# Kernel tuning notes

Measured on AMD Instinct MI355X. Metric: run time of the kernel, lower is better.

## Reference

```python
import jax, jax.numpy as jnp
import numpy as np

D = 1024      # d_model
E = 8         # initial_experts
H = 4 * D     # expert FFN hidden
CAP_F = 1.25  # capacity_factor
VOCAB = 256


def setup_inputs() -> dict:
    key = jax.random.key(0)
    ks = jax.random.split(key, 10)
    w = lambda k, shape, s: jax.random.normal(k, shape, jnp.float32) * s
    return dict(
        byte_seq=jax.random.randint(ks[0], (4, 2048), 0, VOCAB, jnp.int32),
        emb=w(ks[1], (VOCAB, D), 0.02),
        Wp=w(ks[2], (D, D), 1.0 / np.sqrt(D)), bp=jnp.zeros((D,), jnp.float32),
        Wg=w(ks[3], (D, D), 1.0 / np.sqrt(D)), bg=jnp.zeros((D,), jnp.float32),
        Wr=w(ks[4], (D, E), 1.0 / np.sqrt(D)), br=jnp.zeros((E,), jnp.float32),
        W1=w(ks[5], (E, D, H), 1.0 / np.sqrt(D)), b1=jnp.zeros((E, H), jnp.float32),
        W2=w(ks[6], (E, H, D), 1.0 / np.sqrt(H)), b2=jnp.zeros((E, D), jnp.float32),
        Wh=w(ks[7], (D, VOCAB), 1.0 / np.sqrt(D)), bh=jnp.zeros((VOCAB,), jnp.float32),
    )


def reference(byte_seq, emb, Wp, bp, Wg, bg, Wr, br, W1, b1, W2, b2, Wh, bh):
    # ---- byte embedding ----
    x = emb[byte_seq]                                 # [B,T,D]
    B, T, _ = x.shape

    # ---- SSM core: precompute input projections, scan only the recurrence ----
    px = x @ Wp + bp                                   # [B,T,D]
    gx = jax.nn.sigmoid(x @ Wg + bg)                   # [B,T,D]

    def step(state, inp):
        p, g = inp
        state = jnp.tanh(p + state)
        return state, g * state

    s0 = jnp.zeros((B, D), x.dtype)
    next_state, ys = jax.lax.scan(step, s0, (px.transpose(1, 0, 2), gx.transpose(1, 0, 2)))
    y = ys.transpose(1, 0, 2)                          # [B,T,D]

    # ---- capacity-limited top-1 MoE routing ----
    xf = y.reshape(-1, D)                              # [N,D]
    N = xf.shape[0]
    probs = jax.nn.softmax(xf @ Wr + br, axis=-1)      # [N,E]
    top = jnp.argmax(probs, axis=-1)                   # [N]
    onehot = jax.nn.one_hot(top, E, dtype=xf.dtype)    # [N,E]
    pos = jnp.cumsum(onehot, axis=0) * onehot          # 1-based slot within expert
    capacity = int(CAP_F * N / E)
    keep = (pos > 0) & (pos <= capacity)               # [N,E] tokens within capacity
    gate = jnp.take_along_axis(probs, top[:, None], axis=-1)[:, 0]  # [N]
    scale = gate * keep.any(axis=-1).astype(xf.dtype)

    # grouped expert FFN (fixed small loop over experts, masked combine)
    out = jnp.zeros_like(xf)
    for e in range(E):
        h = jax.nn.gelu(xf @ W1[e] + b1[e])            # [N,H]
        oe = h @ W2[e] + b2[e]                         # [N,D]
        out = out + oe * keep[:, e].astype(xf.dtype)[:, None]
    out = out * scale[:, None]

    entropy_loss = -jnp.mean(jnp.sum(probs * jnp.log(probs + 1e-9), axis=-1))
    expert_counts = jnp.sum(onehot, axis=0)

    logits = out.reshape(B, T, D) @ Wh + bh            # [B,T,256]
    return logits, next_state, entropy_loss, expert_counts
```

## Files before the change

kernel.cpp:

```cpp
#include <hip/hip_runtime.h>
#include <hip/hip_bf16.h>
#include <cstdint>
#include <cstddef>

#define AS1 __attribute__((address_space(1)))
#define AS3 __attribute__((address_space(3)))

typedef __hip_bfloat16 bf16;
typedef float f32x4 __attribute__((ext_vector_type(4)));
typedef short bf16x8 __attribute__((ext_vector_type(8)));

#define B_     4
#define T_     2048
#define D_     1024
#define E_     8
#define H_     4096
#define NTOK   8192
#define CAP    1280
#define VOCAB_ 256

static constexpr size_t OFF_PG    = 0;
static constexpr size_t OFF_Y     = 2097152;
static constexpr size_t OFF_TOP   = 35651584;
static constexpr size_t OFF_GATE  = 35684352;
static constexpr size_t OFF_ENT   = 35717120;
static constexpr size_t OFF_CNT   = 35749888;
static constexpr size_t OFF_CKEPT = 35750144;
static constexpr size_t OFF_SLOT  = 35750400;
static constexpr size_t OFF_XE    = 35791360;
static constexpr size_t OFF_HE    = 56762880;
static constexpr size_t OFF_WT    = 140648960;
static constexpr size_t OFF_WHT   = 207757824;
static constexpr size_t OFF_OUTB  = 208282112;

#define LOGITS_OFF 0
#define NS_OFF     2097152
#define ENT_OFF    2101248
#define CNT_OFF    2101249

__device__ __forceinline__ void gll16(const void* g, void* l) {
  __builtin_amdgcn_global_load_lds((AS1 const void*)g, (AS3 void*)l, 16, 0, 0);
}
__device__ __forceinline__ unsigned short f2bu(float f) {
  bf16 h = __float2bfloat16(f);
  return __builtin_bit_cast(unsigned short, h);
}
__device__ __forceinline__ float bu2f(unsigned short u) {
  unsigned int x = ((unsigned int)u) << 16;
  return __builtin_bit_cast(float, x);
}
__device__ __forceinline__ float fast_tanh(float z) {
  float e2 = __expf(z + z);
  return fmaf(-2.f, __builtin_amdgcn_rcpf(e2 + 1.f), 1.f);
}

__global__ __launch_bounds__(256) void slv_embproj_part(
    const float* __restrict__ emb, const float* __restrict__ Wp,
    const float* __restrict__ Wg,
    float* __restrict__ Ppart, float* __restrict__ Gpart) {
  __shared__ float embT[128][9];
  int rb = blockIdx.x, kc = blockIdx.y;
  int r0 = rb * 8, k0 = kc * 128;
  int tid = threadIdx.x;
  int c = tid * 4;
  {
    int i4 = tid * 4;
    int r = i4 >> 7, kb = i4 & 127;
    f32x4 v = *reinterpret_cast<const f32x4*>(emb + (size_t)(r0 + r) * D_ + k0 + kb);
    embT[kb + 0][r] = v.x; embT[kb + 1][r] = v.y;
    embT[kb + 2][r] = v.z; embT[kb + 3][r] = v.w;
  }
  __syncthreads();
  f32x4 aP[8] = {}, aG[8] = {};
  #pragma unroll 4
  for (int kk = 0; kk < 128; ++kk) {
    f32x4 wp = *reinterpret_cast<const f32x4*>(Wp + (size_t)(k0 + kk) * D_ + c);
    f32x4 wg = *reinterpret_cast<const f32x4*>(Wg + (size_t)(k0 + kk) * D_ + c);
    #pragma unroll
    for (int r = 0; r < 8; ++r) {
      float e = embT[kk][r];
      aP[r] += e * wp;
      aG[r] += e * wg;
    }
  }
  #pragma unroll
  for (int r = 0; r < 8; ++r) {
    size_t o = ((size_t)kc * 256 + r0 + r) * D_ + c;
    *reinterpret_cast<f32x4*>(Ppart + o) = aP[r];
    *reinterpret_cast<f32x4*>(Gpart + o) = aG[r];
  }
}

__global__ __launch_bounds__(256) void slv_embproj_reduce(
    const float* __restrict__ Ppart, const float* __restrict__ Gpart,
    const float* __restrict__ bp, const float* __restrict__ bg,
    float2* __restrict__ PG) {
  int i = blockIdx.x * 256 + threadIdx.x;
  int r = i >> 8;
  int c = (i & 255) * 4;
  f32x4 sp = {}, sg = {};
  #pragma unroll
  for (int kc = 0; kc < 8; ++kc) {
    size_t o = ((size_t)kc * 256 + r) * D_ + c;
    sp += *reinterpret_cast<const f32x4*>(Ppart + o);
    sg += *reinterpret_cast<const f32x4*>(Gpart + o);
  }
  sp += *reinterpret_cast<const f32x4*>(bp + c);
  sg += *reinterpret_cast<const f32x4*>(bg + c);
  f32x4 g;
  g.x = 1.f / (1.f + __expf(-sg.x));
  g.y = 1.f / (1.f + __expf(-sg.y));
  g.z = 1.f / (1.f + __expf(-sg.z));
  g.w = 1.f / (1.f + __expf(-sg.w));
  f32x4 st0 = { sp.x, g.x, sp.y, g.y };
  f32x4 st1 = { sp.z, g.z, sp.w, g.w };
  f32x4* dst = reinterpret_cast<f32x4*>(PG + (size_t)r * D_ + c);
  dst[0] = st0; dst[1] = st1;
}

__global__ __launch_bounds__(256) void slv_gatherpg(
    const int* __restrict__ bytes, const float2* __restrict__ PG,
    float2* __restrict__ pg_seq) {
  int t0 = blockIdx.x * 16;
  __shared__ int bl[16];
  if (threadIdx.x < 16) bl[threadIdx.x] = bytes[t0 + threadIdx.x];
  __syncthreads();
  int c = threadIdx.x * 4;
  #pragma unroll 4
  for (int u = 0; u < 16; ++u) {
    const f32x4* src = (const f32x4*)(PG + (size_t)bl[u] * D_ + c);
    f32x4* dst = (f32x4*)(pg_seq + (size_t)(t0 + u) * D_ + c);
    f32x4 v0 = src[0], v1 = src[1];
    dst[0] = v0; dst[1] = v1;
  }
}

#define SU 16
__global__ __launch_bounds__(64, 1) void slv_scan(
    const float2* __restrict__ pg_seq,
    float* __restrict__ y, float* __restrict__ ns) {
  int b = blockIdx.x >> 4;
  int d = (blockIdx.x & 15) * 64 + threadIdx.x;
  const float2* pp = pg_seq + (size_t)b * T_ * D_ + d;
  float* yp = y + (size_t)b * T_ * D_ + d;
  float2 pA[SU], pB[SU];
  #pragma unroll
  for (int u = 0; u < SU; ++u) pA[u] = pp[(size_t)u * D_];
  float s = 0.f;
  for (int t0 = 0; t0 < T_; t0 += 2 * SU) {
    #pragma unroll
    for (int u = 0; u < SU; ++u) pB[u] = pp[(size_t)(t0 + SU + u) * D_];
    #pragma unroll
    for (int u = 0; u < SU; ++u) {
      s = fast_tanh(pA[u].x + s);
      yp[(size_t)(t0 + u) * D_] = pA[u].y * s;
    }
    if (t0 + 2 * SU < T_) {
      #pragma unroll
      for (int u = 0; u < SU; ++u) pA[u] = pp[(size_t)(t0 + 2 * SU + u) * D_];
    }
    #pragma unroll
    for (int u = 0; u < SU; ++u) {
      s = fast_tanh(pB[u].x + s);
      yp[(size_t)(t0 + SU + u) * D_] = pB[u].y * s;
    }
  }
  ns[b * D_ + d] = s;
}

__global__ __launch_bounds__(256) void slv_router(
    const float* __restrict__ y, const float* __restrict__ Wr, const float* __restrict__ br,
    int* __restrict__ top, float* __restrict__ gate, float* __restrict__ entTok,
    int* __restrict__ countsInt) {
  int wave = threadIdx.x >> 6, lane = threadIdx.x & 63;
  int tok = blockIdx.x * 4 + wave;
  const float* yr = y + (size_t)tok * D_;
  float acc[E_];
  #pragma unroll
  for (int e = 0; e < E_; ++e) acc[e] = 0.f;
  for (int i = 0; i < 16; ++i) {
    int d = i * 64 + lane;
    float v = yr[d];
    const float4* w = (const float4*)(Wr + d * E_);
    float4 w0 = w[0], w1 = w[1];
    acc[0] = fmaf(v, w0.x, acc[0]); acc[1] = fmaf(v, w0.y, acc[1]);
    acc[2] = fmaf(v, w0.z, acc[2]); acc[3] = fmaf(v, w0.w, acc[3]);
    acc[4] = fmaf(v, w1.x, acc[4]); acc[5] = fmaf(v, w1.y, acc[5]);
    acc[6] = fmaf(v, w1.z, acc[6]); acc[7] = fmaf(v, w1.w, acc[7]);
  }
  #pragma unroll
  for (int off = 32; off; off >>= 1)
    #pragma unroll
    for (int e = 0; e < E_; ++e) acc[e] += __shfl_xor(acc[e], off);
  if (lane == 0) {
    float l[E_], p[E_];
    float mx = -1e30f;
    #pragma unroll
    for (int e = 0; e < E_; ++e) { l[e] = acc[e] + br[e]; mx = fmaxf(mx, l[e]); }
    float sum = 0.f;
    #pragma unroll
    for (int e = 0; e < E_; ++e) { p[e] = expf(l[e] - mx); sum += p[e]; }
    float inv = 1.f / sum;
    int bestE = 0; float bestP = -1.f; float ent = 0.f;
    #pragma unroll
    for (int e = 0; e < E_; ++e) {
      float pe = p[e] * inv;
      ent += pe * logf(pe + 1e-9f);
      if (pe > bestP) { bestP = pe; bestE = e; }
    }
    top[tok] = bestE; gate[tok] = bestP; entTok[tok] = ent;
    atomicAdd(&countsInt[bestE], 1);
  }
}

__global__ __launch_bounds__(256) void slv_capacity(
    const int* __restrict__ top, int* __restrict__ slotTok, int* __restrict__ cntKept) {
  __shared__ unsigned char tops[NTOK];
  __shared__ unsigned int wt[4][4];
  int tid = threadIdx.x, lane = tid & 63, w = tid >> 6;
  for (int i = tid; i < NTOK; i += 256) tops[i] = (unsigned char)top[i];
  __syncthreads();
  unsigned int c0 = 0, c1 = 0, c2 = 0, c3 = 0;
  int n0 = tid * 32;
  for (int i = 0; i < 32; ++i) {
    int v = tops[n0 + i];
    unsigned inc = 1u << ((v & 1) << 4);
    int hi = v >> 1;
    if (hi == 0) c0 += inc;
    else if (hi == 1) c1 += inc;
    else if (hi == 2) c2 += inc;
    else c3 += inc;
  }
  unsigned int s0 = c0, s1 = c1, s2 = c2, s3 = c3;
  #pragma unroll
  for (int off = 1; off < 64; off <<= 1) {
    unsigned int t0 = (unsigned)__shfl_up((int)s0, off);
    unsigned int t1 = (unsigned)__shfl_up((int)s1, off);
    unsigned int t2 = (unsigned)__shfl_up((int)s2, off);
    unsigned int t3 = (unsigned)__shfl_up((int)s3, off);
    if (lane >= off) { s0 += t0; s1 += t1; s2 += t2; s3 += t3; }
  }
  if (lane == 63) { wt[w][0] = s0; wt[w][1] = s1; wt[w][2] = s2; wt[w][3] = s3; }
  __syncthreads();
  unsigned int p0 = 0, p1 = 0, p2 = 0, p3 = 0;
  for (int i = 0; i < w; ++i) { p0 += wt[i][0]; p1 += wt[i][1]; p2 += wt[i][2]; p3 += wt[i][3]; }
  unsigned int e0 = s0 - c0 + p0, e1 = s1 - c1 + p1, e2 = s2 - c2 + p2, e3 = s3 - c3 + p3;
  int base[E_];
  base[0] = e0 & 0xffff; base[1] = e0 >> 16;
  base[2] = e1 & 0xffff; base[3] = e1 >> 16;
  base[4] = e2 & 0xffff; base[5] = e2 >> 16;
  base[6] = e3 & 0xffff; base[7] = e3 >> 16;
  if (tid == 0) {
    unsigned int t0t = wt[0][0] + wt[1][0] + wt[2][0] + wt[3][0];
    unsigned int t1t = wt[0][1] + wt[1][1] + wt[2][1] + wt[3][1];
    unsigned int t2t = wt[0][2] + wt[1][2] + wt[2][2] + wt[3][2];
    unsigned int t3t = wt[0][3] + wt[1][3] + wt[2][3] + wt[3][3];
    cntKept[0] = min((int)(t0t & 0xffff), CAP); cntKept[1] = min((int)(t0t >> 16), CAP);
    cntKept[2] = min((int)(t1t & 0xffff), CAP); cntKept[3] = min((int)(t1t >> 16), CAP);
    cntKept[4] = min((int)(t2t & 0xffff), CAP); cntKept[5] = min((int)(t2t >> 16), CAP);
    cntKept[6] = min((int)(t3t & 0xffff), CAP); cntKept[7] = min((int)(t3t >> 16), CAP);
  }
  for (int i = 0; i < 32; ++i) {
    int n = n0 + i;
    int v = tops[n];
    #pragma unroll
    for (int e = 0; e < E_; ++e) {
      if (v == e) {
        int r = base[e]++;
        if (r < CAP) slotTok[e * CAP + r] = n;
      }
    }
  }
}

__global__ __launch_bounds__(256) void slv_gather(
    const float* __restrict__ y, const int* __restrict__ slotTok,
    const int* __restrict__ cntKept, unsigned short* __restrict__ Xe) {
  int slot = blockIdx.x;
  int e = slot / CAP, r = slot % CAP;
  int c4 = threadIdx.x * 4;
  ushort4 o;
  if (r < cntKept[e]) {
    int tok = slotTok[slot];
    float4 v = *(const float4*)(y + (size_t)tok * D_ + c4);
    o.x = f2bu(v.x); o.y = f2bu(v.y); o.z = f2bu(v.z); o.w = f2bu(v.w);
  } else {
    o.x = 0; o.y = 0; o.z = 0; o.w = 0;
  }
  *(ushort4*)(Xe + (size_t)slot * D_ + c4) = o;
}

__global__ __launch_bounds__(256) void slv_transpose(
    const float* __restrict__ in, bf16* __restrict__ out, int R, int C) {
  __shared__ float tile[64][65];
  size_t mat = (size_t)blockIdx.z * R * C;
  int c0 = blockIdx.x * 64, r0 = blockIdx.y * 64;
  int tid = threadIdx.x;
  #pragma unroll
  for (int j = 0; j < 16; ++j) {
    int idx = j * 256 + tid; int r = idx >> 6, c = idx & 63;
    tile[r][c] = in[mat + (size_t)(r0 + r) * C + c0 + c];
  }
  __syncthreads();
  #pragma unroll
  for (int j = 0; j < 4; ++j) {
    int lin = j * 256 + tid;
    int cc = lin >> 4;
    int rr = (lin & 15) * 4;
    ushort4 v;
    v.x = f2bu(tile[rr + 0][cc]); v.y = f2bu(tile[rr + 1][cc]);
    v.z = f2bu(tile[rr + 2][cc]); v.w = f2bu(tile[rr + 3][cc]);
    *(ushort4*)((unsigned short*)out + mat + (size_t)(c0 + cc) * R + r0 + rr) = v;
  }
}

__device__ __forceinline__ void gemm_core(
    const char* ga, const char* gb, int K, bf16* As, bf16* Bs,
    f32x4 (&acc)[4][4], int wave, int lane, int wr, int wc) {
  const int Krow = K * 2;
  for (int ks = 0; ks < K; ks += 64) {
    #pragma unroll
    for (int rnd = 0; rnd < 4; ++rnd) {
      int chunk = rnd * 4 + wave;
      int o = chunk * 1024 + lane * 16;
      int row = o >> 7, col = o & 127;
      int scol = col ^ ((row & 7) << 4);
      size_t gofs = (size_t)row * Krow + (size_t)ks * 2 + scol;
      gll16(ga + gofs, (char*)As + chunk * 1024);
      gll16(gb + gofs, (char*)Bs + chunk * 1024);
    }
    __syncthreads();
    #pragma unroll
    for (int kk = 0; kk < 2; ++kk) {
      bf16x8 a[4], b[4];
      int koff = kk * 64 + ((lane >> 4) << 4);
      #pragma unroll
      for (int m = 0; m < 4; ++m) {
        int row = wr * 64 + m * 16 + (lane & 15);
        int sc = koff ^ ((row & 7) << 4);
        a[m] = *(const bf16x8*)((const char*)As + row * 128 + sc);
      }
      #pragma unroll
      for (int n = 0; n < 4; ++n) {
        int row = wc * 64 + n * 16 + (lane & 15);
        int sc = koff ^ ((row & 7) << 4);
        b[n] = *(const bf16x8*)((const char*)Bs + row * 128 + sc);
      }
      #pragma unroll
      for (int m = 0; m < 4; ++m)
        #pragma unroll
        for (int n = 0; n < 4; ++n)
          acc[m][n] = __builtin_amdgcn_mfma_f32_16x16x32_bf16(a[m], b[n], acc[m][n], 0, 0, 0);
    }
    __syncthreads();
  }
}

__device__ __forceinline__ void gemm256_8p(
    const char* ga, const char* gb, size_t krow, size_t kbyte0, int NH,
    char* lds, int tid, int lane, int wr, int wc, f32x4 (&acc)[8][4]) {
  auto STG = [&](int h, int r) {
    int o = (r & 1) * 8192 + tid * 16;
    int l = o >> 7, rem = o & 127;
    int rem2 = rem ^ ((l & 7) << 4);
    int row = 2 * l + (rem2 >> 6);
    int kb = rem2 & 63;
    const char* g = (r < 2) ? ga : gb;
    size_t gofs = (size_t)row * krow + kbyte0 + (size_t)h * 64 + kb;
    gll16(g + gofs, lds + (h & 3) * 32768 + ((r < 2) ? 0 : 16384) + o);
  };
  int l15 = lane & 15;
  int lhalf = l15 >> 1;
  int aoff = (((lane & 1) << 6) | ((lane >> 4) << 4)) ^ (lhalf << 4);
  STG(0, 0); STG(0, 1); STG(0, 2); STG(0, 3);
  STG(1, 0); STG(1, 1); STG(1, 2); STG(1, 3);
  STG(2, 0); STG(2, 1); STG(2, 2); STG(2, 3);
  asm volatile("s_waitcnt vmcnt(8)" ::: "memory");
  __builtin_amdgcn_s_barrier();
  for (int h = 0; h < NH; ++h) {
    const char* Ab = lds + (h & 3) * 32768;
    const char* Bb = Ab + 16384;
    bf16x8 a[4], b[4];
    #pragma unroll
    for (int n = 0; n < 4; ++n)
      b[n] = *(const bf16x8*)(Bb + 128 * (wc * 32 + n * 8 + lhalf) + aoff);
    #pragma unroll
    for (int m = 0; m < 4; ++m)
      a[m] = *(const bf16x8*)(Ab + 128 * (wr * 64 + m * 8 + lhalf) + aoff);
    if (h + 3 < NH) { STG(h + 3, 0); STG(h + 3, 1); }
    __builtin_amdgcn_s_barrier();
    asm volatile("s_waitcnt lgkmcnt(0)" ::: "memory");
    __builtin_amdgcn_sched_barrier(0);
    __builtin_amdgcn_s_setprio(1);
    #pragma unroll
    for (int m = 0; m < 4; ++m)
      #pragma unroll
      for (int n = 0; n < 4; ++n)
        acc[m][n] = __builtin_amdgcn_mfma_f32_16x16x32_bf16(a[m], b[n], acc[m][n], 0, 0, 0);
    __builtin_amdgcn_s_setprio(0);
    __builtin_amdgcn_s_barrier();
    #pragma unroll
    for (int m = 0; m < 4; ++m)
      a[m] = *(const bf16x8*)(Ab + 128 * (wr * 64 + (m + 4) * 8 + lhalf) + aoff);
    if (h + 3 < NH) { STG(h + 3, 2); STG(h + 3, 3); }
    if (h + 3 <= NH - 1)      asm volatile("s_waitcnt vmcnt(8)" ::: "memory");
    else if (h + 2 == NH - 1) asm volatile("s_waitcnt vmcnt(4)" ::: "memory");
    else if (h + 1 == NH - 1) asm volatile("s_waitcnt vmcnt(0)" ::: "memory");
    __builtin_amdgcn_s_barrier();
    asm volatile("s_waitcnt lgkmcnt(0)" ::: "memory");
    __builtin_amdgcn_sched_barrier(0);
    __builtin_amdgcn_s_setprio(1);
    #pragma unroll
    for (int m = 0; m < 4; ++m)
      #pragma unroll
      for (int n = 0; n < 4; ++n)
        acc[m + 4][n] = __builtin_amdgcn_mfma_f32_16x16x32_bf16(a[m], b[n], acc[m + 4][n], 0, 0, 0);
    __builtin_amdgcn_s_setprio(0);
    __builtin_amdgcn_s_barrier();
  }
}

__global__ __launch_bounds__(512, 2) void slv_ffn1_g(
    const bf16* __restrict__ Xe, const bf16* __restrict__ W1t, const float* __restrict__ b1,
    const int* __restrict__ cntKept, unsigned short* __restrict__ He) {
  int e = blockIdx.z, mt = blockIdx.y, nt = blockIdx.x;
  if (mt * 256 >= cntKept[e]) return;
  extern __shared__ char lds[];
  int tid = threadIdx.x, wave = tid >> 6, lane = tid & 63;
  int wr = wave >> 2, wc = wave & 3;
  const char* ga = (const char*)(Xe + ((size_t)e * CAP + mt * 256) * D_);
  const char* gb = (const char*)(W1t + ((size_t)e * H_ + nt * 256) * D_);
  f32x4 acc[8][4] = {};
  gemm256_8p(ga, gb, (size_t)D_ * 2, 0, D_ / 32, lds, tid, lane, wr, wc, acc);
  size_t slot0 = (size_t)e * CAP + mt * 256;
  int colb = nt * 256 + wc * 64;
  #pragma unroll
  for (int m = 0; m < 8; ++m) {
    int trow0 = wr * 128 + m * 16 + ((lane >> 4) << 2);
    #pragma unroll
    for (int n = 0; n < 4; ++n) {
      int col = colb + n * 16 + (lane & 15);
      float bias = b1[e * H_ + col];
      #pragma unroll
      for (int r = 0; r < 4; ++r) {
        float x = acc[m][n][r] + bias;
        float t = fast_tanh(0.7978845608028654f * (x + 0.044715f * x * x * x));
        float gel = 0.5f * x * (1.f + t);
        He[(slot0 + trow0 + r) * (size_t)H_ + col] = f2bu(gel);
      }
    }
  }
}

__global__ __launch_bounds__(512, 2) void slv_ffn2_part(
    const bf16* __restrict__ He, const bf16* __restrict__ W2t,
    const int* __restrict__ cntKept,
    unsigned short* __restrict__ part0, unsigned short* __restrict__ part1) {
  int ez = blockIdx.z;
  int e = ez >> 1, s = ez & 1;
  int mt = blockIdx.y, nt = blockIdx.x;
  if (mt * 256 >= cntKept[e]) return;
  extern __shared__ char lds[];
  int tid = threadIdx.x, wave = tid >> 6, lane = tid & 63;
  int wr = wave >> 2, wc = wave & 3;
  const char* ga = (const char*)(He + ((size_t)e * CAP + mt * 256) * H_);
  const char* gb = (const char*)(W2t + ((size_t)e * D_ + nt * 256) * H_);
  f32x4 acc[8][4] = {};
  gemm256_8p(ga, gb, (size_t)H_ * 2, (size_t)s * 2048 * 2, 2048 / 32,
             lds, tid, lane, wr, wc, acc);
  unsigned short* part = s ? part1 : part0;
  size_t slot0 = (size_t)e * CAP + mt * 256;
  int colb = nt * 256 + wc * 64;
  #pragma unroll
  for (int m = 0; m < 8; ++m) {
    int trow0 = wr * 128 + m * 16 + ((lane >> 4) << 2);
    #pragma unroll
    for (int n = 0; n < 4; ++n) {
      int col = colb + n * 16 + (lane & 15);
      #pragma unroll
      for (int r = 0; r < 4; ++r)
        part[(slot0 + trow0 + r) * (size_t)D_ + col] = f2bu(acc[m][n][r]);
    }
  }
}

__global__ __launch_bounds__(256) void slv_ffn2_reduce(
    const unsigned short* __restrict__ part0, const unsigned short* __restrict__ part1,
    const float* __restrict__ b2, const int* __restrict__ cntKept,
    const int* __restrict__ slotTok, const float* __restrict__ gate,
    unsigned short* __restrict__ outb) {
  int slot = blockIdx.x;
  int e = slot / CAP, r = slot % CAP;
  if (r >= cntKept[e]) return;
  int tok = slotTok[slot];
  float sc = gate[tok];
  int c4 = threadIdx.x * 4;
  ushort4 p0 = *(const ushort4*)(part0 + (size_t)slot * D_ + c4);
  ushort4 p1 = *(const ushort4*)(part1 + (size_t)slot * D_ + c4);
  const float4 bb = *(const float4*)(b2 + e * D_ + c4);
  ushort4 o;
  o.x = f2bu((bu2f(p0.x) + bu2f(p1.x) + bb.x) * sc);
  o.y = f2bu((bu2f(p0.y) + bu2f(p1.y) + bb.y) * sc);
  o.z = f2bu((bu2f(p0.z) + bu2f(p1.z) + bb.z) * sc);
  o.w = f2bu((bu2f(p0.w) + bu2f(p1.w) + bb.w) * sc);
  *(ushort4*)(outb + (size_t)tok * D_ + c4) = o;
}

__global__ __launch_bounds__(256) void slv_head(
    const bf16* __restrict__ outb, const bf16* __restrict__ Wht, const float* __restrict__ bh,
    float* __restrict__ logits) {
  int nt = blockIdx.x, mt = blockIdx.y;
  __shared__ __align__(16) bf16 As[128 * 64], Bs[128 * 64];
  int tid = threadIdx.x, wave = tid >> 6, lane = tid & 63;
  int wr = wave >> 1, wc = wave & 1;
  const char* ga = (const char*)(outb + (size_t)mt * 128 * D_);
  const char* gb = (const char*)(Wht + (size_t)nt * 128 * D_);
  f32x4 acc[4][4] = {};
  gemm_core(ga, gb, D_, As, Bs, acc, wave, lane, wr, wc);
  int colb = nt * 128 + wc * 64;
  #pragma unroll
  for (int m = 0; m < 4; ++m) {
    int trow0 = wr * 64 + m * 16 + ((lane >> 4) << 2);
    #pragma unroll
    for (int n = 0; n < 4; ++n) {
      int col = colb + n * 16 + (lane & 15);
      float bias = bh[col];
      #pragma unroll
      for (int r = 0; r < 4; ++r) {
        int row = mt * 128 + trow0 + r;
        logits[(size_t)row * VOCAB_ + col] = acc[m][n][r] + bias;
      }
    }
  }
}

__global__ __launch_bounds__(256) void slv_finalize(
    const float* __restrict__ entTok, const int* __restrict__ countsInt,
    float* __restrict__ out) {
  __shared__ float red[256];
  int tid = threadIdx.x;
  float s = 0.f;
  for (int i = tid; i < NTOK; i += 256) s += entTok[i];
  red[tid] = s;
  __syncthreads();
  for (int off = 128; off; off >>= 1) {
    if (tid < off) red[tid] += red[tid + off];
    __syncthreads();
  }
  if (tid == 0) out[ENT_OFF] = -red[0] / (float)NTOK;
  if (tid < E_) out[CNT_OFF + tid] = (float)countsInt[tid];
}

extern "C" void kernel_launch(void* const* d_in, const int* in_sizes, int n_in,
                              void* d_out, int out_size, void* d_ws, size_t ws_size,
                              hipStream_t stream) {
  (void)in_sizes; (void)n_in; (void)out_size; (void)ws_size;
  const int*   byte_seq = (const int*)d_in[0];
  const float* emb = (const float*)d_in[1];
  const float* Wp  = (const float*)d_in[2];
  const float* bp  = (const float*)d_in[3];
  const float* Wg  = (const float*)d_in[4];
  const float* bg  = (const float*)d_in[5];
  const float* Wr  = (const float*)d_in[6];
  const float* br  = (const float*)d_in[7];
  const float* W1  = (const float*)d_in[8];
  const float* b1  = (const float*)d_in[9];
  const float* W2  = (const float*)d_in[10];
  const float* b2  = (const float*)d_in[11];
  const float* Wh  = (const float*)d_in[12];
  const float* bh  = (const float*)d_in[13];
  float* out = (float*)d_out;

  char* ws = (char*)d_ws;
  float2* PG      = (float2*)(ws + OFF_PG);
  float* y        = (float*)(ws + OFF_Y);
  int*   top      = (int*)(ws + OFF_TOP);
  float* gate     = (float*)(ws + OFF_GATE);
  float* entTok   = (float*)(ws + OFF_ENT);
  int*   countsInt= (int*)(ws + OFF_CNT);
  int*   cntKept  = (int*)(ws + OFF_CKEPT);
  int*   slotTok  = (int*)(ws + OFF_SLOT);
  unsigned short* Xe  = (unsigned short*)(ws + OFF_XE);
  unsigned short* He  = (unsigned short*)(ws + OFF_HE);
  bf16*  Wt       = (bf16*)(ws + OFF_WT);
  bf16*  Wht      = (bf16*)(ws + OFF_WHT);
  unsigned short* outb = (unsigned short*)(ws + OFF_OUTB);
  float*  Ppart   = (float*)(ws + OFF_HE);
  float*  Gpart   = (float*)(ws + OFF_HE + 8388608);
  float2* pg_seq  = (float2*)(ws + OFF_HE);
  unsigned short* part0 = (unsigned short*)(ws + OFF_Y);
  unsigned short* part1 = (unsigned short*)(ws + OFF_XE);

  hipFuncSetAttribute(reinterpret_cast<const void*>(slv_ffn1_g),
                      hipFuncAttributeMaxDynamicSharedMemorySize, 131072);
  hipFuncSetAttribute(reinterpret_cast<const void*>(slv_ffn2_part),
                      hipFuncAttributeMaxDynamicSharedMemorySize, 131072);

  hipMemsetAsync(countsInt, 0, E_ * sizeof(int), stream);
  hipMemsetAsync(outb, 0, (size_t)NTOK * D_ * 2, stream);

  slv_embproj_part<<<dim3(32, 8), 256, 0, stream>>>(emb, Wp, Wg, Ppart, Gpart);
  slv_embproj_reduce<<<256, 256, 0, stream>>>(Ppart, Gpart, bp, bg, PG);
  slv_gatherpg<<<NTOK / 16, 256, 0, stream>>>(byte_seq, PG, pg_seq);
  slv_scan<<<64, 64, 0, stream>>>(pg_seq, y, out + NS_OFF);
  slv_router<<<NTOK / 4, 256, 0, stream>>>(y, Wr, br, top, gate, entTok, countsInt);
  slv_capacity<<<1, 256, 0, stream>>>(top, slotTok, cntKept);
  slv_gather<<<E_ * CAP, 256, 0, stream>>>(y, slotTok, cntKept, Xe);

  slv_transpose<<<dim3(4, 16, 1), 256, 0, stream>>>(Wh, Wht, 1024, 256);
  slv_transpose<<<dim3(64, 16, 8), 256, 0, stream>>>(W1, Wt, 1024, 4096);
  slv_ffn1_g<<<dim3(16, 5, 8), 512, 131072, stream>>>((const bf16*)Xe, Wt, b1, cntKept, He);
  slv_transpose<<<dim3(16, 64, 8), 256, 0, stream>>>(W2, Wt, 4096, 1024);
  slv_ffn2_part<<<dim3(4, 5, 16), 512, 131072, stream>>>((const bf16*)He, Wt, cntKept, part0, part1);
  slv_ffn2_reduce<<<E_ * CAP, 256, 0, stream>>>(part0, part1, b2, cntKept, slotTok, gate, outb);
  slv_head<<<dim3(2, 64), 256, 0, stream>>>((const bf16*)outb, Wht, bh, out + LOGITS_OFF);
  slv_finalize<<<1, 256, 0, stream>>>(entTok, countsInt, out);
}
```

Baseline: 570.5 us.

## Overlap weight transposes with scan and shrink expert GEMM tiles to 128 rows

Folds the Wh and W1 transposes into the scan launch as extra blocks, so the idle GPU during the latency-bound 16-block sequential scan does transpose work in parallel. The scan now uses 16 blocks of 256 threads instead of 64 blocks of 64. The expert FFN GEMMs move from 256x256 tiles with a 4-stage buffer to 128x256 tiles with a 3-stage buffer and less LDS, allowing more blocks per CU and finer skipping of empty capacity rows. The trade-off is less data reuse per tile, and the scan's wave layout changes, which may affect its latency.

```diff
diff --git a/kernel.cpp b/kernel.cpp
--- a/kernel.cpp
+++ b/kernel.cpp
@@ -135,12 +135,48 @@
   }
 }
 
+__device__ __forceinline__ void transpose_tile(
+    const float* __restrict__ in, bf16* __restrict__ out, int R, int C,
+    int bx, int by, int bz, int tid) {
+  __shared__ float tile[64][65];
+  size_t mat = (size_t)bz * R * C;
+  int c0 = bx * 64, r0 = by * 64;
+  #pragma unroll
+  for (int j = 0; j < 16; ++j) {
+    int idx = j * 256 + tid; int r = idx >> 6, c = idx & 63;
+    tile[r][c] = in[mat + (size_t)(r0 + r) * C + c0 + c];
+  }
+  __syncthreads();
+  #pragma unroll
+  for (int j = 0; j < 4; ++j) {
+    int lin = j * 256 + tid;
+    int cc = lin >> 4;
+    int rr = (lin & 15) * 4;
+    ushort4 v;
+    v.x = f2bu(tile[rr + 0][cc]); v.y = f2bu(tile[rr + 1][cc]);
+    v.z = f2bu(tile[rr + 2][cc]); v.w = f2bu(tile[rr + 3][cc]);
+    *(ushort4*)((unsigned short*)out + mat + (size_t)(c0 + cc) * R + r0 + rr) = v;
+  }
+}
+
 #define SU 16
-__global__ __launch_bounds__(64, 1) void slv_scan(
-    const float2* __restrict__ pg_seq,
-    float* __restrict__ y, float* __restrict__ ns) {
-  int b = blockIdx.x >> 4;
-  int d = (blockIdx.x & 15) * 64 + threadIdx.x;
+__global__ __launch_bounds__(256, 1) void slv_scan_trans(
+    const float2* __restrict__ pg_seq, float* __restrict__ y, float* __restrict__ ns,
+    const float* __restrict__ W1, bf16* __restrict__ W1t,
+    const float* __restrict__ Wh, bf16* __restrict__ Wht) {
+  int bid = blockIdx.x, tid = threadIdx.x;
+  if (bid >= 16) {
+    if (bid < 80) {
+      int blk = bid - 16;
+      transpose_tile(Wh, Wht, 1024, 256, blk & 3, blk >> 2, 0, tid);
+    } else {
+      int blk = bid - 80;
+      transpose_tile(W1, W1t, 1024, 4096, blk & 63, (blk >> 6) & 15, blk >> 10, tid);
+    }
+    return;
+  }
+  int b = bid >> 2;
+  int d = (bid & 3) * 256 + tid;
   const float2* pp = pg_seq + (size_t)b * T_ * D_ + d;
   float* yp = y + (size_t)b * T_ * D_ + d;
   float2 pA[SU], pB[SU];
@@ -292,26 +328,7 @@
 
 __global__ __launch_bounds__(256) void slv_transpose(
     const float* __restrict__ in, bf16* __restrict__ out, int R, int C) {
-  __shared__ float tile[64][65];
-  size_t mat = (size_t)blockIdx.z * R * C;
-  int c0 = blockIdx.x * 64, r0 = blockIdx.y * 64;
-  int tid = threadIdx.x;
-  #pragma unroll
-  for (int j = 0; j < 16; ++j) {
-    int idx = j * 256 + tid; int r = idx >> 6, c = idx & 63;
-    tile[r][c] = in[mat + (size_t)(r0 + r) * C + c0 + c];
-  }
-  __syncthreads();
-  #pragma unroll
-  for (int j = 0; j < 4; ++j) {
-    int lin = j * 256 + tid;
-    int cc = lin >> 4;
-    int rr = (lin & 15) * 4;
-    ushort4 v;
-    v.x = f2bu(tile[rr + 0][cc]); v.y = f2bu(tile[rr + 1][cc]);
-    v.z = f2bu(tile[rr + 2][cc]); v.w = f2bu(tile[rr + 3][cc]);
-    *(ushort4*)((unsigned short*)out + mat + (size_t)(c0 + cc) * R + r0 + rr) = v;
-  }
+  transpose_tile(in, out, R, C, blockIdx.x, blockIdx.y, blockIdx.z, threadIdx.x);
 }
 
 __device__ __forceinline__ void gemm_core(
@@ -356,39 +373,40 @@
   }
 }
 
-__device__ __forceinline__ void gemm256_8p(
+__device__ __forceinline__ void gemm_hp(
     const char* ga, const char* gb, size_t krow, size_t kbyte0, int NH,
-    char* lds, int tid, int lane, int wr, int wc, f32x4 (&acc)[8][4]) {
+    char* lds, int tid, int lane, int wr, int wc, f32x4 (&acc)[4][4]) {
   auto STG = [&](int h, int r) {
-    int o = (r & 1) * 8192 + tid * 16;
+    int o = (r == 0) ? (tid * 16) : ((r - 1) * 8192 + tid * 16);
     int l = o >> 7, rem = o & 127;
     int rem2 = rem ^ ((l & 7) << 4);
     int row = 2 * l + (rem2 >> 6);
     int kb = rem2 & 63;
-    const char* g = (r < 2) ? ga : gb;
+    const char* g = (r == 0) ? ga : gb;
     size_t gofs = (size_t)row * krow + kbyte0 + (size_t)h * 64 + kb;
-    gll16(g + gofs, lds + (h & 3) * 32768 + ((r < 2) ? 0 : 16384) + o);
+    gll16(g + gofs, lds + (h % 3) * 24576 + ((r == 0) ? 0 : 8192) + o);
   };
-  int l15 = lane & 15;
-  int lhalf = l15 >> 1;
+  int lhalf = (lane & 15) >> 1;
   int aoff = (((lane & 1) << 6) | ((lane >> 4) << 4)) ^ (lhalf << 4);
-  STG(0, 0); STG(0, 1); STG(0, 2); STG(0, 3);
-  STG(1, 0); STG(1, 1); STG(1, 2); STG(1, 3);
-  STG(2, 0); STG(2, 1); STG(2, 2); STG(2, 3);
-  asm volatile("s_waitcnt vmcnt(8)" ::: "memory");
+  STG(0, 0); STG(0, 1); STG(0, 2);
+  STG(1, 0); STG(1, 1); STG(1, 2);
+  asm volatile("s_waitcnt vmcnt(3)" ::: "memory");
   __builtin_amdgcn_s_barrier();
   for (int h = 0; h < NH; ++h) {
-    const char* Ab = lds + (h & 3) * 32768;
-    const char* Bb = Ab + 16384;
+    const char* Ab = lds + (h % 3) * 24576;
+    const char* Bb = Ab + 8192;
     bf16x8 a[4], b[4];
+    #pragma unroll
+    for (int m = 0; m < 4; ++m)
+      a[m] = *(const bf16x8*)(Ab + 128 * (wr * 32 + m * 8 + lhalf) + aoff);
     #pragma unroll
     for (int n = 0; n < 4; ++n)
       b[n] = *(const bf16x8*)(Bb + 128 * (wc * 32 + n * 8 + lhalf) + aoff);
-    #pragma unroll
-    for (int m = 0; m < 4; ++m)
-      a[m] = *(const bf16x8*)(Ab + 128 * (wr * 64 + m * 8 + lhalf) + aoff);
-    if (h + 3 < NH) { STG(h + 3, 0); STG(h + 3, 1); }
-    __builtin_amdgcn_s_barrier();
+    if (h + 2 < NH) { STG(h + 2, 0); STG(h + 2, 1); STG(h + 2, 2); }
+    if (h + 1 < NH) {
+      if (h + 2 < NH) asm volatile("s_waitcnt vmcnt(3)" ::: "memory");
+      else            asm volatile("s_waitcnt vmcnt(0)" ::: "memory");
+    }
     asm volatile("s_waitcnt lgkmcnt(0)" ::: "memory");
     __builtin_amdgcn_sched_barrier(0);
     __builtin_amdgcn_s_setprio(1);
@@ -399,44 +417,26 @@
         acc[m][n] = __builtin_amdgcn_mfma_f32_16x16x32_bf16(a[m], b[n], acc[m][n], 0, 0, 0);
     __builtin_amdgcn_s_setprio(0);
     __builtin_amdgcn_s_barrier();
-    #pragma unroll
-    for (int m = 0; m < 4; ++m)
-      a[m] = *(const bf16x8*)(Ab + 128 * (wr * 64 + (m + 4) * 8 + lhalf) + aoff);
-    if (h + 3 < NH) { STG(h + 3, 2); STG(h + 3, 3); }
-    if (h + 3 <= NH - 1)      asm volatile("s_waitcnt vmcnt(8)" ::: "memory");
-    else if (h + 2 == NH - 1) asm volatile("s_waitcnt vmcnt(4)" ::: "memory");
-    else if (h + 1 == NH - 1) asm volatile("s_waitcnt vmcnt(0)" ::: "memory");
-    __builtin_amdgcn_s_barrier();
-    asm volatile("s_waitcnt lgkmcnt(0)" ::: "memory");
-    __builtin_amdgcn_sched_barrier(0);
-    __builtin_amdgcn_s_setprio(1);
-    #pragma unroll
-    for (int m = 0; m < 4; ++m)
-      #pragma unroll
-      for (int n = 0; n < 4; ++n)
-        acc[m + 4][n] = __builtin_amdgcn_mfma_f32_16x16x32_bf16(a[m], b[n], acc[m + 4][n], 0, 0, 0);
-    __builtin_amdgcn_s_setprio(0);
-    __builtin_amdgcn_s_barrier();
-  }
-}
-
-__global__ __launch_bounds__(512, 2) void slv_ffn1_g(
+  }
+}
+
+__global__ __launch_bounds__(512, 4) void slv_ffn1_hp(
     const bf16* __restrict__ Xe, const bf16* __restrict__ W1t, const float* __restrict__ b1,
     const int* __restrict__ cntKept, unsigned short* __restrict__ He) {
   int e = blockIdx.z, mt = blockIdx.y, nt = blockIdx.x;
-  if (mt * 256 >= cntKept[e]) return;
+  if (mt * 128 >= cntKept[e]) return;
   extern __shared__ char lds[];
   int tid = threadIdx.x, wave = tid >> 6, lane = tid & 63;
   int wr = wave >> 2, wc = wave & 3;
-  const char* ga = (const char*)(Xe + ((size_t)e * CAP + mt * 256) * D_);
+  const char* ga = (const char*)(Xe + ((size_t)e * CAP + mt * 128) * D_);
   const char* gb = (const char*)(W1t + ((size_t)e * H_ + nt * 256) * D_);
-  f32x4 acc[8][4] = {};
-  gemm256_8p(ga, gb, (size_t)D_ * 2, 0, D_ / 32, lds, tid, lane, wr, wc, acc);
-  size_t slot0 = (size_t)e * CAP + mt * 256;
+  f32x4 acc[4][4] = {};
+  gemm_hp(ga, gb, (size_t)D_ * 2, 0, D_ / 32, lds, tid, lane, wr, wc, acc);
+  size_t slot0 = (size_t)e * CAP + mt * 128;
   int colb = nt * 256 + wc * 64;
   #pragma unroll
-  for (int m = 0; m < 8; ++m) {
-    int trow0 = wr * 128 + m * 16 + ((lane >> 4) << 2);
+  for (int m = 0; m < 4; ++m) {
+    int trow0 = wr * 64 + m * 16 + ((lane >> 4) << 2);
     #pragma unroll
     for (int n = 0; n < 4; ++n) {
       int col = colb + n * 16 + (lane & 15);
@@ -452,28 +452,28 @@
   }
 }
 
-__global__ __launch_bounds__(512, 2) void slv_ffn2_part(
+__global__ __launch_bounds__(512, 4) void slv_ffn2_hp(
     const bf16* __restrict__ He, const bf16* __restrict__ W2t,
     const int* __restrict__ cntKept,
     unsigned short* __restrict__ part0, unsigned short* __restrict__ part1) {
   int ez = blockIdx.z;
   int e = ez >> 1, s = ez & 1;
   int mt = blockIdx.y, nt = blockIdx.x;
-  if (mt * 256 >= cntKept[e]) return;
+  if (mt * 128 >= cntKept[e]) return;
   extern __shared__ char lds[];
   int tid = threadIdx.x, wave = tid >> 6, lane = tid & 63;
   int wr = wave >> 2, wc = wave & 3;
-  const char* ga = (const char*)(He + ((size_t)e * CAP + mt * 256) * H_);
+  const char* ga = (const char*)(He + ((size_t)e * CAP + mt * 128) * H_);
   const char* gb = (const char*)(W2t + ((size_t)e * D_ + nt * 256) * H_);
-  f32x4 acc[8][4] = {};
-  gemm256_8p(ga, gb, (size_t)H_ * 2, (size_t)s * 2048 * 2, 2048 / 32,
-             lds, tid, lane, wr, wc, acc);
+  f32x4 acc[4][4] = {};
+  gemm_hp(ga, gb, (size_t)H_ * 2, (size_t)s * 2048 * 2, 2048 / 32,
+          lds, tid, lane, wr, wc, acc);
   unsigned short* part = s ? part1 : part0;
-  size_t slot0 = (size_t)e * CAP + mt * 256;
+  size_t slot0 = (size_t)e * CAP + mt * 128;
   int colb = nt * 256 + wc * 64;
   #pragma unroll
-  for (int m = 0; m < 8; ++m) {
-    int trow0 = wr * 128 + m * 16 + ((lane >> 4) << 2);
+  for (int m = 0; m < 4; ++m) {
+    int trow0 = wr * 64 + m * 16 + ((lane >> 4) << 2);
     #pragma unroll
     for (int n = 0; n < 4; ++n) {
       int col = colb + n * 16 + (lane & 15);
@@ -591,10 +591,10 @@
   unsigned short* part0 = (unsigned short*)(ws + OFF_Y);
   unsigned short* part1 = (unsigned short*)(ws + OFF_XE);
 
-  hipFuncSetAttribute(reinterpret_cast<const void*>(slv_ffn1_g),
-                      hipFuncAttributeMaxDynamicSharedMemorySize, 131072);
-  hipFuncSetAttribute(reinterpret_cast<const void*>(slv_ffn2_part),
-                      hipFuncAttributeMaxDynamicSharedMemorySize, 131072);
+  hipFuncSetAttribute(reinterpret_cast<const void*>(slv_ffn1_hp),
+                      hipFuncAttributeMaxDynamicSharedMemorySize, 73728);
+  hipFuncSetAttribute(reinterpret_cast<const void*>(slv_ffn2_hp),
+                      hipFuncAttributeMaxDynamicSharedMemorySize, 73728);
 
   hipMemsetAsync(countsInt, 0, E_ * sizeof(int), stream);
   hipMemsetAsync(outb, 0, (size_t)NTOK * D_ * 2, stream);
@@ -602,16 +602,15 @@
   slv_embproj_part<<<dim3(32, 8), 256, 0, stream>>>(emb, Wp, Wg, Ppart, Gpart);
   slv_embproj_reduce<<<256, 256, 0, stream>>>(Ppart, Gpart, bp, bg, PG);
   slv_gatherpg<<<NTOK / 16, 256, 0, stream>>>(byte_seq, PG, pg_seq);
-  slv_scan<<<64, 64, 0, stream>>>(pg_seq, y, out + NS_OFF);
+  slv_scan_trans<<<16 + 64 + 8192, 256, 0, stream>>>(pg_seq, y, out + NS_OFF,
+                                                     W1, Wt, Wh, Wht);
   slv_router<<<NTOK / 4, 256, 0, stream>>>(y, Wr, br, top, gate, entTok, countsInt);
   slv_capacity<<<1, 256, 0, stream>>>(top, slotTok, cntKept);
   slv_gather<<<E_ * CAP, 256, 0, stream>>>(y, slotTok, cntKept, Xe);
 
-  slv_transpose<<<dim3(4, 16, 1), 256, 0, stream>>>(Wh, Wht, 1024, 256);
-  slv_transpose<<<dim3(64, 16, 8), 256, 0, stream>>>(W1, Wt, 1024, 4096);
-  slv_ffn1_g<<<dim3(16, 5, 8), 512, 131072, stream>>>((const bf16*)Xe, Wt, b1, cntKept, He);
+  slv_ffn1_hp<<<dim3(16, 10, 8), 512, 73728, stream>>>((const bf16*)Xe, Wt, b1, cntKept, He);
   slv_transpose<<<dim3(16, 64, 8), 256, 0, stream>>>(W2, Wt, 4096, 1024);
-  slv_ffn2_part<<<dim3(4, 5, 16), 512, 131072, stream>>>((const bf16*)He, Wt, cntKept, part0, part1);
+  slv_ffn2_hp<<<dim3(4, 10, 16), 512, 73728, stream>>>((const bf16*)He, Wt, cntKept, part0, part1);
   slv_ffn2_reduce<<<E_ * CAP, 256, 0, stream>>>(part0, part1, b2, cntKept, slotTok, gate, outb);
   slv_head<<<dim3(2, 64), 256, 0, stream>>>((const bf16*)outb, Wht, bh, out + LOGITS_OFF);
   slv_finalize<<<1, 256, 0, stream>>>(entTok, countsInt, out);
```

Result: slower. 623.3 us (+9.3%).
